# Optimization experiments

Measured on AMD Instinct MI355X. Metric: run time of the kernel, lower is better.

The kernel has to match this reference:

```python
import jax, jax.numpy as jnp
import numpy as np

NUM_HEADS = 16
KEEP_RATIO = 0.25
BETA = 1.0
EPS = 1e-6


def setup_inputs() -> dict:
    key = jax.random.key(0)
    ks = jax.random.split(key, 5)
    B, N, C = 16, 577, 1024
    x = jax.random.normal(ks[0], (B, N, C), dtype=jnp.float32)
    qkv_w = jax.random.normal(ks[1], (3 * C, C), dtype=jnp.float32) * (C ** -0.5)
    proj_w = jax.random.normal(ks[2], (C, C), dtype=jnp.float32) * (C ** -0.5)
    proj_b = jax.random.normal(ks[3], (C,), dtype=jnp.float32)
    # visit counts per (head, key); uniform positive
    ucb_count_score = jax.random.uniform(ks[4], (NUM_HEADS, N), dtype=jnp.float32) * 100.0
    return {"x": x, "qkv_w": qkv_w, "proj_w": proj_w, "proj_b": proj_b,
            "ucb_count_score": ucb_count_score, "counter": 100, "ucb_enabled": 1}


def reference(x, qkv_w, proj_w, proj_b, ucb_count_score, counter, ucb_enabled):
    B, N, C = x.shape
    H = NUM_HEADS
    Dh = C // H
    scale = Dh ** -0.5

    qkv = (x @ qkv_w.T).reshape(B, N, 3, H, Dh).transpose(2, 0, 3, 1, 4)  # [3,B,H,N,Dh]
    q, k, v = qkv[0], qkv[1], qkv[2]
    attn_scores = jnp.einsum('bhqd,bhkd->bhqk', q, k) * scale  # [B,H,N,N]

    score_delta = None
    if ucb_enabled and counter > 50:
        # exclude_cls=True: prune only over keys 1..N-1
        nkeys = N - 1
        kk = max(1, int(nkeys * KEEP_RATIO))
        scores_for_topk = attn_scores[..., 1:]                      # [B,H,N,nkeys]
        cnt = ucb_count_score[:, 1:]                                # [H,nkeys]
        expl = BETA * jnp.sqrt(jnp.log(counter + 1.0) / (cnt + EPS))  # [H,nkeys]
        ucb_scores = scores_for_topk + expl[None, :, None, :]
        # top-k mask via flat scatter
        flat = ucb_scores.reshape(-1, nkeys)
        _, top_idx = jax.lax.top_k(flat, kk)                        # [BHN, kk]
        rows = jnp.arange(flat.shape[0])[:, None]
        mask = jnp.zeros(flat.shape, dtype=bool).at[rows, top_idx].set(True)
        mask = mask.reshape(B, H, N, nkeys)
        cls_mask = jnp.ones((B, H, N, 1), dtype=bool)
        mask_full = jnp.concatenate([cls_mask, mask], axis=-1)      # [B,H,N,N]
        neg = -jnp.finfo(attn_scores.dtype).max
        pruned = jnp.where(mask_full, attn_scores, neg)
        attn_probs = jax.nn.softmax(pruned, axis=-1)
        score_delta = mask_full.sum(axis=(0, 2)).astype(jnp.int32)  # [H,N]
    else:
        attn_probs = jax.nn.softmax(attn_scores, axis=-1)

    context = jnp.einsum('bhqk,bhkd->bhqd', attn_probs, v)
    out = context.transpose(0, 2, 1, 3).reshape(B, N, C) @ proj_w.T + proj_b
    return (out, score_delta)
```

## Files before the change

### kernel.cpp

```cpp
#include <hip/hip_runtime.h>
#include <hip/hip_bf16.h>

#define B_ 16
#define N_ 577
#define C_ 1024
#define H_ 16
#define DH_ 64
#define M_ (B_*N_)
#define KKEEP 144
#define VTP 584
#define SST 325

typedef __attribute__((ext_vector_type(8))) short bf16x8;
typedef __attribute__((ext_vector_type(4))) float f32x4;

__device__ __forceinline__ float b2f(unsigned short u){ return __uint_as_float(((unsigned int)u) << 16); }
__device__ __forceinline__ unsigned short f2bu(float f){
  __hip_bfloat16 h = __float2bfloat16(f);
  return *(unsigned short*)&h;
}
__device__ __forceinline__ float wredmaxf(float v){
  #pragma unroll
  for (int m=1;m<64;m<<=1) v = fmaxf(v, __shfl_xor(v, m, 64));
  return v;
}
__device__ __forceinline__ float wredsumf(float v){
  #pragma unroll
  for (int m=1;m<64;m<<=1) v += __shfl_xor(v, m, 64);
  return v;
}

__global__ __launch_bounds__(256) void cvt_bf16(
    const float* __restrict__ X, const float* __restrict__ Wq, const float* __restrict__ Wp,
    unsigned short* __restrict__ xb, unsigned short* __restrict__ wqb, unsigned short* __restrict__ wpb)
{
  size_t g = (size_t)blockIdx.x*256 + threadIdx.x;
  const float* src; unsigned short* dst; size_t off;
  if (g < 1181696){ src = X; dst = xb; off = g*8; }
  else if (g < 1574912){ src = Wq; dst = wqb; off = (g-1181696)*8; }
  else { src = Wp; dst = wpb; off = (g-1574912)*8; }
  float4 a = *(const float4*)(src+off), b = *(const float4*)(src+off+4);
  unsigned short t[8] = { f2bu(a.x), f2bu(a.y), f2bu(a.z), f2bu(a.w),
                          f2bu(b.x), f2bu(b.y), f2bu(b.z), f2bu(b.w) };
  *(uint4*)(dst+off) = *(uint4*)t;
}

__global__ __launch_bounds__(256) void gemm_qkv_mfma(
    const unsigned short* __restrict__ Xb, const unsigned short* __restrict__ Wb,
    unsigned short* __restrict__ qb, unsigned short* __restrict__ kb,
    unsigned short* __restrict__ vb)
{
  __shared__ unsigned short As[128][40];
  __shared__ unsigned short Bs[128][40];
  const int tid = threadIdx.x;
  const int lane = tid & 63, wave = tid >> 6;
  const int wm = wave >> 1, wn = wave & 1;
  const int lr = lane & 15, kh = lane >> 4;
  const int bm = blockIdx.x*128, bn = blockIdx.y*128;
  const int srow = tid >> 1, shalf = tid & 1;

  f32x4 acc[4][4];
  #pragma unroll
  for (int i=0;i<4;++i)
    #pragma unroll
    for (int j=0;j<4;++j) acc[i][j] = (f32x4){0.f,0.f,0.f,0.f};

  const int m_s = bm + srow;
  for (int k0=0; k0<1024; k0+=32){
    __syncthreads();
    {
      uint4 a0={0,0,0,0}, a1={0,0,0,0};
      if (m_s < M_){
        const uint4* s = (const uint4*)(Xb + (size_t)m_s*1024 + k0 + shalf*16);
        a0 = s[0]; a1 = s[1];
      }
      *(uint4*)&As[srow][shalf*16]   = a0;
      *(uint4*)&As[srow][shalf*16+8] = a1;
      const uint4* sw = (const uint4*)(Wb + (size_t)(bn+srow)*1024 + k0 + shalf*16);
      *(uint4*)&Bs[srow][shalf*16]   = sw[0];
      *(uint4*)&Bs[srow][shalf*16+8] = sw[1];
    }
    __syncthreads();
    bf16x8 af[4], bfr[4];
    #pragma unroll
    for (int f=0; f<4; ++f){
      af[f]  = *(const bf16x8*)&As[wm*64 + f*16 + lr][kh*8];
      bfr[f] = *(const bf16x8*)&Bs[wn*64 + f*16 + lr][kh*8];
    }
    #pragma unroll
    for (int fm=0; fm<4; ++fm)
      #pragma unroll
      for (int fn=0; fn<4; ++fn)
        acc[fm][fn] = __builtin_amdgcn_mfma_f32_16x16x32_bf16(af[fm], bfr[fn], acc[fm][fn], 0,0,0);
  }
  #pragma unroll
  for (int fm=0; fm<4; ++fm){
    #pragma unroll
    for (int j=0; j<4; ++j){
      int m = bm + wm*64 + fm*16 + kh*4 + j;
      if (m >= M_) continue;
      int b = m / N_, n = m - b*N_;
      #pragma unroll
      for (int fn=0; fn<4; ++fn){
        int c = bn + wn*64 + fn*16 + lr;
        int three = c >> 10, hh = (c >> 6) & 15, dd = c & 63;
        size_t off = ((size_t)(b*H_ + hh)*N_ + n)*DH_ + dd;
        unsigned short val = f2bu(acc[fm][fn][j]);
        if (three == 0)      qb[off] = val;
        else if (three == 1) kb[off] = val;
        else                 vb[off] = val;
      }
    }
  }
}

__global__ __launch_bounds__(256) void transpose_v(
    const unsigned short* __restrict__ vb, unsigned short* __restrict__ vt)
{
  __shared__ unsigned short tile[64][72];
  const int t = threadIdx.x;
  const int bh = blockIdx.x / 10, nt = blockIdx.x % 10;
  const int n0 = nt*64;
  {
    int r = t >> 2, c0 = (t & 3) * 16;
    int n = n0 + r;
    uint4 a0={0,0,0,0}, a1={0,0,0,0};
    if (n < N_){
      const uint4* s = (const uint4*)(vb + ((size_t)bh*N_ + n)*DH_ + c0);
      a0 = s[0]; a1 = s[1];
    }
    *(uint4*)&tile[r][c0]   = a0;
    *(uint4*)&tile[r][c0+8] = a1;
  }
  __syncthreads();
  {
    int d = t & 63, j0 = (t >> 6) * 16;
    unsigned short v[16];
    #pragma unroll
    for (int i=0;i<16;++i) v[i] = tile[j0+i][d];
    unsigned short* dst = vt + ((size_t)bh*DH_ + d)*VTP + n0 + j0;
    if (n0 + j0 + 15 <= VTP-1){
      *(uint4*)dst     = *(uint4*)&v[0];
      *(uint4*)(dst+8) = *(uint4*)&v[8];
    } else if (n0 + j0 + 7 <= VTP-1){
      *(uint4*)dst = *(uint4*)&v[0];
    }
  }
}

__global__ __launch_bounds__(256,6) void attn_kernel(
    const unsigned short* __restrict__ qw, const unsigned short* __restrict__ kw,
    const unsigned short* __restrict__ vt,
    const float* __restrict__ ucb, const int* __restrict__ counter_p,
    unsigned short* __restrict__ ctx, int* __restrict__ delta)
{
  __shared__ __align__(16) float S[16][SST];
  __shared__ float expl_s[584];
  __shared__ int   cnt_s[584];
  unsigned short (*pus)[584] = (unsigned short (*)[584])&S[0][0];

  const int tid = threadIdx.x;
  const int lane = tid & 63, wave = tid >> 6;
  const int lr = lane & 15, kh = lane >> 4;
  const int blk = blockIdx.x;
  const int bh = blk / 37, tileq = blk % 37;
  const int h = bh & 15;
  const int row0 = tileq * 16;

  const float logc = logf((float)(*counter_p) + 1.0f);
  for (int k2=tid; k2<N_; k2+=256){
    cnt_s[k2] = 0;
    expl_s[k2] = (k2==0) ? 0.f : sqrtf(logc / (ucb[h*N_ + k2] + 1e-6f));
  }

  const unsigned short* qbb = qw + (size_t)bh*N_*DH_;
  const unsigned short* kbb = kw + (size_t)bh*N_*DH_;
  bf16x8 aq0 = {0,0,0,0,0,0,0,0}, aq1 = {0,0,0,0,0,0,0,0};
  {
    int qr = row0 + lr;
    if (qr < N_){
      aq0 = *(const bf16x8*)(qbb + (size_t)qr*DH_ + kh*8);
      aq1 = *(const bf16x8*)(qbb + (size_t)qr*DH_ + 32 + kh*8);
    }
  }

  float acc[4][10];
  #pragma unroll
  for (int r=0;r<4;++r)
    #pragma unroll
    for (int s=0;s<10;++s) acc[r][s]=0.f;

  #pragma unroll
  for (int half=0; half<2; ++half){
    const int t0 = half ? 20 : 0, t1 = half ? 37 : 20, keyoff = half*320;
    for (int tile = t0 + wave; tile < t1; tile += 4){
      int keyr = tile*16 + lr;
      bf16x8 b0 = {0,0,0,0,0,0,0,0}, b1 = {0,0,0,0,0,0,0,0};
      if (keyr < N_){
        b0 = *(const bf16x8*)(kbb + (size_t)keyr*DH_ + kh*8);
        b1 = *(const bf16x8*)(kbb + (size_t)keyr*DH_ + 32 + kh*8);
      }
      f32x4 d = (f32x4){0.f,0.f,0.f,0.f};
      d = __builtin_amdgcn_mfma_f32_16x16x32_bf16(aq0, b0, d, 0,0,0);
      d = __builtin_amdgcn_mfma_f32_16x16x32_bf16(aq1, b1, d, 0,0,0);
      int col = tile*16 - keyoff + lr;
      #pragma unroll
      for (int rg=0; rg<4; ++rg)
        S[kh*4+rg][col] = d[rg];
    }
    __syncthreads();
    #pragma unroll
    for (int s=0; s<5; ++s){
      int sg = half*5 + s;
      int k = sg*64 + lane;
      if (k < N_){
        #pragma unroll
        for (int r=0;r<4;++r) acc[r][sg] = S[wave*4+r][k - keyoff];
      }
    }
    __syncthreads();
  }

  #pragma unroll
  for (int r=0;r<4;++r){
    const int lrow = wave*4 + r;
    const int n = row0 + lrow;
    const bool rv = (n < N_);
    float sc[10], uv[10]; bool vd[10];
    #pragma unroll
    for (int s=0;s<10;++s) sc[s] = acc[r][s]*0.125f;
    float mx0 = -3.4e38f, mn0 = 3.4e38f;
    #pragma unroll
    for (int s=0;s<10;++s){
      int k = s*64 + lane;
      vd[s] = (k >= 1) && (k < N_);
      uv[s] = sc[s] + (k < N_ ? expl_s[k] : 0.f);
      if (vd[s]){ mx0 = fmaxf(mx0, uv[s]); mn0 = fminf(mn0, uv[s]); }
    }
    const float mx1 = wredmaxf(mx0);
    const float mn1 = -wredmaxf(-mn0);
    const float scale = 1022.f / fmaxf(mx1 - mn1, 1e-30f);
    unsigned uq[10];
    #pragma unroll
    for (int s=0;s<10;++s)
      uq[s] = vd[s] ? (1u + (unsigned)((uv[s]-mn1)*scale)) : 0u;

    unsigned T = 0u;
    for (int bit=9; bit>=0; --bit){
      unsigned cand = T | (1u << bit);
      int c = 0;
      #pragma unroll
      for (int s=0;s<10;++s) c += (int)__popcll(__ballot(uq[s] >= cand));
      if (c >= KKEEP) T = cand;
    }
    int cgt = 0;
    #pragma unroll
    for (int s=0;s<10;++s) cgt += (int)__popcll(__ballot(uq[s] > T));
    const int rem = KKEEP - cgt;
    unsigned long long em[10];
    #pragma unroll
    for (int s=0;s<10;++s) em[s] = __ballot(uq[s] == T);
    const unsigned long long below = lane ? (~0ull >> (64 - lane)) : 0ull;
    bool keep[10];
    int pref = 0;
    #pragma unroll
    for (int s=0;s<10;++s){
      int k = s*64 + lane;
      bool kp2 = false;
      if (k == 0) kp2 = true;
      else if (k < N_){
        if (uq[s] > T) kp2 = true;
        else if (uq[s] == T) kp2 = (pref + __popcll(em[s] & below)) < rem;
      }
      keep[s] = kp2;
      pref += __popcll(em[s]);
    }
    float mxs = -3.4e38f;
    #pragma unroll
    for (int s=0;s<10;++s) if (keep[s]) mxs = fmaxf(mxs, sc[s]);
    mxs = wredmaxf(mxs);
    float p[10]; float den = 0.f;
    #pragma unroll
    for (int s=0;s<10;++s){ p[s] = keep[s] ? __expf(sc[s]-mxs) : 0.f; den += p[s]; }
    den = wredsumf(den);
    const float inv = 1.0f/den;
    #pragma unroll
    for (int s=0;s<10;++s){
      int k = s*64 + lane;
      if (k < N_) pus[lrow][k] = f2bu(p[s]*inv);
      if (rv && keep[s]) atomicAdd(&cnt_s[k < N_ ? k : 0], 1);
    }
  }
  __syncthreads();

  {
    const int d0 = wave*16;
    const unsigned short* vtb = vt + ((size_t)bh*DH_ + d0 + lr)*VTP;
    f32x4 od = (f32x4){0.f,0.f,0.f,0.f};
    #pragma unroll 3
    for (int kb2=0; kb2<18; ++kb2){
      bf16x8 pa  = *(const bf16x8*)&pus[lr][kb2*32 + kh*8];
      bf16x8 vb8 = *(const bf16x8*)(vtb + kb2*32 + kh*8);
      od = __builtin_amdgcn_mfma_f32_16x16x32_bf16(pa, vb8, od, 0,0,0);
    }
    const float v576 = b2f(vtb[576]);
    #pragma unroll
    for (int rg=0; rg<4; ++rg){
      int q = kh*4 + rg;
      float o = fmaf(b2f(pus[q][576]), v576, od[rg]);
      int n0 = row0 + q;
      if (n0 < N_) ctx[((size_t)bh*N_ + n0)*DH_ + d0 + lr] = f2bu(o);
    }
  }
  __syncthreads();
  for (int k2=tid; k2<N_; k2+=256){
    int c2 = cnt_s[k2];
    if (c2) atomicAdd(&delta[h*N_ + k2], c2);
  }
}

__global__ __launch_bounds__(256) void gemm_proj_mfma(
    const unsigned short* __restrict__ ctxp, const unsigned short* __restrict__ Wb,
    const float* __restrict__ bias, float* __restrict__ out)
{
  __shared__ unsigned short As[128][40];
  __shared__ unsigned short Bs[128][40];
  const int tid = threadIdx.x;
  const int lane = tid & 63, wave = tid >> 6;
  const int wm = wave >> 1, wn = wave & 1;
  const int lr = lane & 15, kh = lane >> 4;
  const int bm = blockIdx.x*128, bn = blockIdx.y*128;
  const int srow = tid >> 1, shalf = tid & 1;

  f32x4 acc[4][4];
  #pragma unroll
  for (int i=0;i<4;++i)
    #pragma unroll
    for (int j=0;j<4;++j) acc[i][j] = (f32x4){0.f,0.f,0.f,0.f};

  const int m_s = bm + srow;
  const int bb = m_s / N_, nn = m_s - bb*N_;

  for (int k0=0; k0<1024; k0+=32){
    __syncthreads();
    {
      uint4 a0 = {0,0,0,0}, a1 = {0,0,0,0};
      if (m_s < M_){
        int hh = k0 >> 6, dd = (k0 & 63) + shalf*16;
        const uint4* s = (const uint4*)(ctxp + ((size_t)(bb*H_ + hh)*N_ + nn)*DH_ + dd);
        a0 = s[0]; a1 = s[1];
      }
      *(uint4*)&As[srow][shalf*16]   = a0;
      *(uint4*)&As[srow][shalf*16+8] = a1;
      const uint4* sw = (const uint4*)(Wb + (size_t)(bn+srow)*1024 + k0 + shalf*16);
      *(uint4*)&Bs[srow][shalf*16]   = sw[0];
      *(uint4*)&Bs[srow][shalf*16+8] = sw[1];
    }
    __syncthreads();
    bf16x8 af[4], bfr[4];
    #pragma unroll
    for (int f=0; f<4; ++f){
      af[f]  = *(const bf16x8*)&As[wm*64 + f*16 + lr][kh*8];
      bfr[f] = *(const bf16x8*)&Bs[wn*64 + f*16 + lr][kh*8];
    }
    #pragma unroll
    for (int fm=0; fm<4; ++fm)
      #pragma unroll
      for (int fn=0; fn<4; ++fn)
        acc[fm][fn] = __builtin_amdgcn_mfma_f32_16x16x32_bf16(af[fm], bfr[fn], acc[fm][fn], 0,0,0);
  }
  float bv[4];
  #pragma unroll
  for (int fn=0; fn<4; ++fn) bv[fn] = bias[bn + wn*64 + fn*16 + lr];
  #pragma unroll
  for (int fm=0; fm<4; ++fm){
    #pragma unroll
    for (int j=0; j<4; ++j){
      int m = bm + wm*64 + fm*16 + kh*4 + j;
      if (m >= M_) continue;
      #pragma unroll
      for (int fn=0; fn<4; ++fn){
        int c = bn + wn*64 + fn*16 + lr;
        out[(size_t)m*1024 + c] = acc[fm][fn][j] + bv[fn];
      }
    }
  }
}

__global__ void delta_to_f32(const int* __restrict__ delta, float* __restrict__ outd){
  int i = blockIdx.x*256 + threadIdx.x;
  if (i < H_*N_) outd[i] = (float)delta[i];
}

extern "C" void kernel_launch(void* const* d_in, const int* in_sizes, int n_in,
                              void* d_out, int out_size, void* d_ws, size_t ws_size,
                              hipStream_t stream) {
  const float* x      = (const float*)d_in[0];
  const float* qkv_w  = (const float*)d_in[1];
  const float* proj_w = (const float*)d_in[2];
  const float* proj_b = (const float*)d_in[3];
  const float* ucb    = (const float*)d_in[4];
  const int*   counter= (const int*)d_in[5];

  float* outO = (float*)d_out;
  float* outD = outO + ((size_t)out_size - (size_t)H_*N_);

  unsigned short* xb  = (unsigned short*)d_ws;
  unsigned short* wqb = xb  + (size_t)M_*C_;
  unsigned short* wpb = wqb + (size_t)3*C_*C_;
  unsigned short* qb  = wpb + (size_t)C_*C_;
  unsigned short* kb  = qb  + (size_t)M_*C_;
  unsigned short* vb  = kb  + (size_t)M_*C_;
  unsigned short* vt  = vb  + (size_t)M_*C_;
  int*         delta  = (int*)(vt + (size_t)B_*H_*DH_*VTP);

  hipMemsetAsync(delta, 0, (size_t)H_*N_*sizeof(int), stream);
  cvt_bf16<<<dim3(6664), 256, 0, stream>>>(x, qkv_w, proj_w, xb, wqb, wpb);
  gemm_qkv_mfma<<<dim3(73,24), 256, 0, stream>>>(xb, wqb, qb, kb, vb);
  transpose_v<<<dim3(2560), 256, 0, stream>>>(vb, vt);
  attn_kernel<<<dim3(256*37), 256, 0, stream>>>(qb, kb, vt, ucb, counter, qb , delta);
  gemm_proj_mfma<<<dim3(73,8), 256, 0, stream>>>(qb, wpb, proj_b, outO);
  delta_to_f32<<<dim3(37), 256, 0, stream>>>(delta, outD);
}
```

Baseline: 378.1 us.

## Use direct global-to-LDS loads in QKV and projection GEMMs

Replaces the register-staged global loads and LDS stores in both GEMM kernels with global_load_lds 16-byte direct transfers into unpadded LDS tiles. This is meant to cut VGPR traffic and instruction count in the tile-loading phase. The out-of-bounds row guard is dropped, so the last M tile reads past the end of the input (the X buffer or the ctx rows), and removing the LDS padding may add bank conflicts on the fragment reads. There is no explicit wait on the asynchronous LDS writes before the barrier, which is a correctness risk.

```diff
diff --git a/kernel.cpp b/kernel.cpp
--- a/kernel.cpp
+++ b/kernel.cpp
@@ -28,6 +28,12 @@
   #pragma unroll
   for (int m=1;m<64;m<<=1) v += __shfl_xor(v, m, 64);
   return v;
+}
+__device__ __forceinline__ void gload16(const unsigned short* g, unsigned short* l){
+  __builtin_amdgcn_global_load_lds(
+      (const __attribute__((address_space(1))) unsigned int*)g,
+      (__attribute__((address_space(3))) unsigned int*)l,
+      16, 0, 0);
 }
 
 __global__ __launch_bounds__(256) void cvt_bf16(
@@ -50,14 +56,33 @@
     unsigned short* __restrict__ qb, unsigned short* __restrict__ kb,
     unsigned short* __restrict__ vb)
 {
-  __shared__ unsigned short As[128][40];
-  __shared__ unsigned short Bs[128][40];
+  __shared__ __align__(16) unsigned short As[128][32];
+  __shared__ __align__(16) unsigned short Bs[128][32];
   const int tid = threadIdx.x;
   const int lane = tid & 63, wave = tid >> 6;
   const int wm = wave >> 1, wn = wave & 1;
   const int lr = lane & 15, kh = lane >> 4;
   const int bm = blockIdx.x*128, bn = blockIdx.y*128;
-  const int srow = tid >> 1, shalf = tid & 1;
+
+  const int idx0 = (wave*2+0)*64 + lane;
+  const int idx1 = (wave*2+1)*64 + lane;
+  const int r0 = idx0 >> 2, c0 = idx0 & 3;
+  const int r1 = idx1 >> 2, c1 = idx1 & 3;
+  const unsigned short* aS0 = Xb + (size_t)(bm + r0)*1024 + c0*8;
+  const unsigned short* aS1 = Xb + (size_t)(bm + r1)*1024 + c1*8;
+  const unsigned short* bS0 = Wb + (size_t)(bn + r0)*1024 + c0*8;
+  const unsigned short* bS1 = Wb + (size_t)(bn + r1)*1024 + c1*8;
+  unsigned short* aD0 = &As[0][0] + (wave*2+0)*512;
+  unsigned short* aD1 = &As[0][0] + (wave*2+1)*512;
+  unsigned short* bD0 = &Bs[0][0] + (wave*2+0)*512;
+  unsigned short* bD1 = &Bs[0][0] + (wave*2+1)*512;
+
+  const unsigned short* aR[4]; const unsigned short* bR[4];
+  #pragma unroll
+  for (int f=0; f<4; ++f){
+    aR[f] = &As[wm*64 + f*16 + lr][kh*8];
+    bR[f] = &Bs[wn*64 + f*16 + lr][kh*8];
+  }
 
   f32x4 acc[4][4];
   #pragma unroll
@@ -65,27 +90,18 @@
     #pragma unroll
     for (int j=0;j<4;++j) acc[i][j] = (f32x4){0.f,0.f,0.f,0.f};
 
-  const int m_s = bm + srow;
   for (int k0=0; k0<1024; k0+=32){
     __syncthreads();
-    {
-      uint4 a0={0,0,0,0}, a1={0,0,0,0};
-      if (m_s < M_){
-        const uint4* s = (const uint4*)(Xb + (size_t)m_s*1024 + k0 + shalf*16);
-        a0 = s[0]; a1 = s[1];
-      }
-      *(uint4*)&As[srow][shalf*16]   = a0;
-      *(uint4*)&As[srow][shalf*16+8] = a1;
-      const uint4* sw = (const uint4*)(Wb + (size_t)(bn+srow)*1024 + k0 + shalf*16);
-      *(uint4*)&Bs[srow][shalf*16]   = sw[0];
-      *(uint4*)&Bs[srow][shalf*16+8] = sw[1];
-    }
+    gload16(aS0 + k0, aD0);
+    gload16(aS1 + k0, aD1);
+    gload16(bS0 + k0, bD0);
+    gload16(bS1 + k0, bD1);
     __syncthreads();
     bf16x8 af[4], bfr[4];
     #pragma unroll
     for (int f=0; f<4; ++f){
-      af[f]  = *(const bf16x8*)&As[wm*64 + f*16 + lr][kh*8];
-      bfr[f] = *(const bf16x8*)&Bs[wn*64 + f*16 + lr][kh*8];
+      af[f]  = *(const bf16x8*)aR[f];
+      bfr[f] = *(const bf16x8*)bR[f];
     }
     #pragma unroll
     for (int fm=0; fm<4; ++fm)
@@ -323,14 +339,36 @@
     const unsigned short* __restrict__ ctxp, const unsigned short* __restrict__ Wb,
     const float* __restrict__ bias, float* __restrict__ out)
 {
-  __shared__ unsigned short As[128][40];
-  __shared__ unsigned short Bs[128][40];
+  __shared__ __align__(16) unsigned short As[128][32];
+  __shared__ __align__(16) unsigned short Bs[128][32];
   const int tid = threadIdx.x;
   const int lane = tid & 63, wave = tid >> 6;
   const int wm = wave >> 1, wn = wave & 1;
   const int lr = lane & 15, kh = lane >> 4;
   const int bm = blockIdx.x*128, bn = blockIdx.y*128;
-  const int srow = tid >> 1, shalf = tid & 1;
+
+  const int idx0 = (wave*2+0)*64 + lane;
+  const int idx1 = (wave*2+1)*64 + lane;
+  const int r0 = idx0 >> 2, c0 = idx0 & 3;
+  const int r1 = idx1 >> 2, c1 = idx1 & 3;
+  const int m0r = bm + r0, m1r = bm + r1;
+  const int b0 = m0r / N_, n0r = m0r - b0*N_;
+  const int b1 = m1r / N_, n1r = m1r - b1*N_;
+  const unsigned short* aBase0 = ctxp + ((size_t)b0*H_*N_ + n0r)*DH_ + c0*8;
+  const unsigned short* aBase1 = ctxp + ((size_t)b1*H_*N_ + n1r)*DH_ + c1*8;
+  const unsigned short* bS0 = Wb + (size_t)(bn + r0)*1024 + c0*8;
+  const unsigned short* bS1 = Wb + (size_t)(bn + r1)*1024 + c1*8;
+  unsigned short* aD0 = &As[0][0] + (wave*2+0)*512;
+  unsigned short* aD1 = &As[0][0] + (wave*2+1)*512;
+  unsigned short* bD0 = &Bs[0][0] + (wave*2+0)*512;
+  unsigned short* bD1 = &Bs[0][0] + (wave*2+1)*512;
+
+  const unsigned short* aR[4]; const unsigned short* bR[4];
+  #pragma unroll
+  for (int f=0; f<4; ++f){
+    aR[f] = &As[wm*64 + f*16 + lr][kh*8];
+    bR[f] = &Bs[wn*64 + f*16 + lr][kh*8];
+  }
 
   f32x4 acc[4][4];
   #pragma unroll
@@ -338,30 +376,19 @@
     #pragma unroll
     for (int j=0;j<4;++j) acc[i][j] = (f32x4){0.f,0.f,0.f,0.f};
 
-  const int m_s = bm + srow;
-  const int bb = m_s / N_, nn = m_s - bb*N_;
-
   for (int k0=0; k0<1024; k0+=32){
     __syncthreads();
-    {
-      uint4 a0 = {0,0,0,0}, a1 = {0,0,0,0};
-      if (m_s < M_){
-        int hh = k0 >> 6, dd = (k0 & 63) + shalf*16;
-        const uint4* s = (const uint4*)(ctxp + ((size_t)(bb*H_ + hh)*N_ + nn)*DH_ + dd);
-        a0 = s[0]; a1 = s[1];
-      }
-      *(uint4*)&As[srow][shalf*16]   = a0;
-      *(uint4*)&As[srow][shalf*16+8] = a1;
-      const uint4* sw = (const uint4*)(Wb + (size_t)(bn+srow)*1024 + k0 + shalf*16);
-      *(uint4*)&Bs[srow][shalf*16]   = sw[0];
-      *(uint4*)&Bs[srow][shalf*16+8] = sw[1];
-    }
+    const size_t hoff = (size_t)(k0 >> 6)*(N_*DH_) + (k0 & 63);
+    gload16(aBase0 + hoff, aD0);
+    gload16(aBase1 + hoff, aD1);
+    gload16(bS0 + k0, bD0);
+    gload16(bS1 + k0, bD1);
     __syncthreads();
     bf16x8 af[4], bfr[4];
     #pragma unroll
     for (int f=0; f<4; ++f){
-      af[f]  = *(const bf16x8*)&As[wm*64 + f*16 + lr][kh*8];
-      bfr[f] = *(const bf16x8*)&Bs[wn*64 + f*16 + lr][kh*8];
+      af[f]  = *(const bf16x8*)aR[f];
+      bfr[f] = *(const bf16x8*)bR[f];
     }
     #pragma unroll
     for (int fm=0; fm<4; ++fm)
```

Measured after the change: 364.0 us. 3.7% less time.
